# Optimization experiments

Measured on AMD Instinct MI355X. Metric: run time of the kernel, lower is better.

Reference implementation:

```python
import jax, jax.numpy as jnp
import numpy as np

DIM = 512; NH = 8; HD = DIM // NH; WS = 28; N = WS * WS; H3 = (DIM * 4) // 3; EPS = 1e-6; B = 16


def _rel_pos_index(H, W):
    # static numpy computation of Swin-style relative position index [N, N]
    coords = np.stack(np.meshgrid(np.arange(H), np.arange(W), indexing='ij')).reshape(2, -1)
    rel = (coords[:, :, None] - coords[:, None, :]).transpose(1, 2, 0)
    rel[..., 0] += H - 1
    rel[..., 1] += W - 1
    rel[..., 0] *= 2 * W - 1
    return rel.sum(-1)

RPI = jnp.asarray(_rel_pos_index(WS, WS))  # [N, N] int


def adaptive_ln(x, w, b, a1w, a1b, a2w, a2b):
    # x: [B,C,H,W]; adapt params from global-avg-pooled 1x1 convs (== matmuls)
    C = x.shape[1]
    pooled = x.mean(axis=(2, 3))                      # [B,C]
    h = jax.nn.relu(pooled @ a1w.T + a1b)             # [B,C/4]
    ad = h @ a2w.T + a2b                              # [B,2C]
    aw = ad[:, :C][:, :, None, None]
    ab = ad[:, C:][:, :, None, None]
    u = x.mean(axis=1, keepdims=True)
    s = ((x - u) ** 2).mean(axis=1, keepdims=True)
    xn = (x - u) * jax.lax.rsqrt(s + EPS)
    return (w[None, :, None, None] * (1.0 + aw)) * xn + (b[None, :, None, None] + ab)


def dwconv(x, w, b):
    y = jax.lax.conv_general_dilated(x, w, (1, 1), 'SAME', feature_group_count=x.shape[1],
                                     dimension_numbers=('NCHW', 'OIHW', 'NCHW'))
    return y + b[None, :, None, None]


def conv1x1(x, w, b):
    return jnp.einsum('bchw,oc->bohw', x, w) + b[None, :, None, None]


def _forward(x, face_priors, n1_w, n1_b, n1_a1w, n1_a1b, n1_a2w, n1_a2b,
             n2_w, n2_b, n2_a1w, n2_a1b, n2_a2w, n2_a2b,
             qkv_w, qkv_b, rpb_table, struct_prior, proj_w, proj_b,
             eye_w, eye_b, nose_w, nose_b, mouth_w, mouth_b,
             fusion_w, fusion_b, gate1_w, gate1_b, gate2_w, gate2_b,
             es1_w, es1_b, es2_w, es2_b, em1_w, em1_b, em2_w, em2_b,
             el1_w, el1_b, el2_w, el2_b, router_w, router_b):
    Bx, C, H, W = x.shape
    n = H * W
    shortcut = x
    xa = adaptive_ln(x, n1_w, n1_b, n1_a1w, n1_a1b, n1_a2w, n1_a2b)
    # --- TripletFaceAttention ---
    xf = xa.reshape(Bx, C, n).transpose(0, 2, 1)                     # [B,N,C]
    qkv = (xf @ qkv_w.T + qkv_b).reshape(Bx, n, 3, NH, HD).transpose(2, 0, 3, 1, 4)
    q, k, v = qkv[0], qkv[1], qkv[2]                                 # [B,h,N,d]
    attn = jnp.einsum('bhnd,bhmd->bhnm', q, k) * (HD ** -0.5)
    attn = attn + struct_prior                                       # learned structure prior [1,h,N,N]
    rpb = rpb_table[RPI]                                             # [N,N,h]
    attn = attn + jnp.transpose(rpb, (2, 0, 1))[None]                # + relative position bias
    attn = attn * face_priors[:, None]                               # multiplicative face mask
    attn = jax.nn.softmax(attn, axis=-1)
    o = jnp.einsum('bhnm,bhmd->bhnd', attn, v).transpose(0, 2, 1, 3).reshape(Bx, n, C)
    o = o @ proj_w.T + proj_b
    x = shortcut + o.transpose(0, 2, 1).reshape(Bx, C, H, W)
    # --- FaceTokenMixer ---
    xn2 = adaptive_ln(x, n2_w, n2_b, n2_a1w, n2_a1b, n2_a2w, n2_a2b)
    cat = jnp.concatenate([dwconv(xn2, eye_w, eye_b),
                           dwconv(xn2, nose_w, nose_b),
                           dwconv(xn2, mouth_w, mouth_b)], axis=1)   # [B,3C,H,W]
    g = jax.nn.sigmoid(conv1x1(jax.nn.relu(conv1x1(xn2, gate1_w, gate1_b)), gate2_w, gate2_b))
    x = x + conv1x1(cat * g, fusion_w, fusion_b)
    # --- EfficientMLP (3-expert MoE, soft routing) ---
    r = jax.nn.softmax(x.mean(axis=(2, 3)) @ router_w.T + router_b, axis=-1)  # [B,3]
    def expert(w1, b1, w2, b2):
        return conv1x1(jax.nn.gelu(conv1x1(x, w1, b1), approximate=False), w2, b2)
    out = (r[:, 0, None, None, None] * expert(es1_w, es1_b, es2_w, es2_b)
           + r[:, 1, None, None, None] * expert(em1_w, em1_b, em2_w, em2_b)
           + r[:, 2, None, None, None] * expert(el1_w, el1_b, el2_w, el2_b))
    return x + out


def setup_inputs() -> dict:
    ks = iter(jax.random.split(jax.random.key(0), 64))
    def rn(shape, s=0.02):
        return jax.random.normal(next(ks), shape, jnp.float32) * s
    d = {}
    d['x'] = jax.random.normal(next(ks), (B, DIM, WS, WS), jnp.float32)
    d['face_priors'] = jax.random.uniform(next(ks), (B, N, N), jnp.float32)
    for p in ('n1', 'n2'):
        d[p + '_w'] = jnp.ones((DIM,), jnp.float32)
        d[p + '_b'] = jnp.zeros((DIM,), jnp.float32)
        d[p + '_a1w'] = rn((DIM // 4, DIM)); d[p + '_a1b'] = jnp.zeros((DIM // 4,), jnp.float32)
        d[p + '_a2w'] = rn((2 * DIM, DIM // 4)); d[p + '_a2b'] = jnp.zeros((2 * DIM,), jnp.float32)
    d['qkv_w'] = rn((3 * DIM, DIM)); d['qkv_b'] = jnp.zeros((3 * DIM,), jnp.float32)
    d['rpb_table'] = rn(((2 * WS - 1) ** 2, NH))
    d['struct_prior'] = rn((1, NH, N, N))
    d['proj_w'] = rn((DIM, DIM)); d['proj_b'] = jnp.zeros((DIM,), jnp.float32)
    d['eye_w'] = rn((DIM, 1, 3, 3)); d['eye_b'] = jnp.zeros((DIM,), jnp.float32)
    d['nose_w'] = rn((DIM, 1, 5, 5)); d['nose_b'] = jnp.zeros((DIM,), jnp.float32)
    d['mouth_w'] = rn((DIM, 1, 7, 7)); d['mouth_b'] = jnp.zeros((DIM,), jnp.float32)
    d['fusion_w'] = rn((DIM, 3 * DIM)); d['fusion_b'] = jnp.zeros((DIM,), jnp.float32)
    d['gate1_w'] = rn((DIM // 4, DIM)); d['gate1_b'] = jnp.zeros((DIM // 4,), jnp.float32)
    d['gate2_w'] = rn((3 * DIM, DIM // 4)); d['gate2_b'] = jnp.zeros((3 * DIM,), jnp.float32)
    for e in ('es', 'em', 'el'):
        d[e + '1_w'] = rn((H3, DIM)); d[e + '1_b'] = jnp.zeros((H3,), jnp.float32)
        d[e + '2_w'] = rn((DIM, H3)); d[e + '2_b'] = jnp.zeros((DIM,), jnp.float32)
    d['router_w'] = rn((3, DIM)); d['router_b'] = jnp.zeros((3,), jnp.float32)
    return d


def reference(x, face_priors, n1_w, n1_b, n1_a1w, n1_a1b, n1_a2w, n1_a2b,
              n2_w, n2_b, n2_a1w, n2_a1b, n2_a2w, n2_a2b,
              qkv_w, qkv_b, rpb_table, struct_prior, proj_w, proj_b,
              eye_w, eye_b, nose_w, nose_b, mouth_w, mouth_b,
              fusion_w, fusion_b, gate1_w, gate1_b, gate2_w, gate2_b,
              es1_w, es1_b, es2_w, es2_b, em1_w, em1_b, em2_w, em2_b,
              el1_w, el1_b, el2_w, el2_b, router_w, router_b):
    return _forward(x, face_priors, n1_w, n1_b, n1_a1w, n1_a1b, n1_a2w, n1_a2b,
                    n2_w, n2_b, n2_a1w, n2_a1b, n2_a2w, n2_a2b,
                    qkv_w, qkv_b, rpb_table, struct_prior, proj_w, proj_b,
                    eye_w, eye_b, nose_w, nose_b, mouth_w, mouth_b,
                    fusion_w, fusion_b, gate1_w, gate1_b, gate2_w, gate2_b,
                    es1_w, es1_b, es2_w, es2_b, em1_w, em1_b, em2_w, em2_b,
                    el1_w, el1_b, el2_w, el2_b, router_w, router_b)
```

## Files before the change

### kernel.cpp

```cpp
#include <hip/hip_runtime.h>
#include <math.h>


#define NPIX 784
#define CDIM 512
#define NHEAD 8
#define C3 1536

typedef unsigned int uint;
typedef unsigned short ushort;
typedef float f32x4 __attribute__((ext_vector_type(4)));
typedef __bf16 bf16x8 __attribute__((ext_vector_type(8)));

#define OFF_XPM ((size_t)0)
#define OFF_W   ((size_t)3211264)
#define OFF_R2  ((size_t)5324288)
#define OFF_VBF ((size_t)14958080)
#define OFF_OBF ((size_t)18169344)
#define OFF_X2  ((size_t)21380608)
#define OFF_X3  ((size_t)27803136)
#define OFF_PL  ((size_t)34225664)
#define OFF_AD  ((size_t)34233856)
#define OFF_RB  ((size_t)34250240)
#define OFF_US  ((size_t)34250288)
#define OFF_RS  ((size_t)34262832)

#define WOFF_QKV 0
#define WOFF_PROJ 786432
#define WOFF_G1  1048576
#define WOFF_G2  1114112
#define WOFF_FUS 1310720
#define WOFF_E1  2097152
#define WOFF_E2  3144704

__device__ __forceinline__ ushort f2bf(float f) {
  unsigned u = __builtin_bit_cast(unsigned, f);
  unsigned r = (u + 0x7fffu + ((u >> 16) & 1u)) >> 16;
  return (ushort)r;
}
__device__ __forceinline__ unsigned pack2bf(float lo, float hi) {
  return (unsigned)f2bf(lo) | ((unsigned)f2bf(hi) << 16);
}
__device__ __forceinline__ float bf2f(ushort u) {
  unsigned x = ((unsigned)u) << 16;
  return __builtin_bit_cast(float, x);
}
__device__ __forceinline__ void unpack4bf(uint2 v, float* o) {
  o[0] = bf2f((ushort)(v.x & 0xffffu)); o[1] = bf2f((ushort)(v.x >> 16));
  o[2] = bf2f((ushort)(v.y & 0xffffu)); o[3] = bf2f((ushort)(v.y >> 16));
}

__global__ __launch_bounds__(64) void pool_mean_k(const float* __restrict__ x,
                                                  float* __restrict__ pooled) {
  int c = blockIdx.x, b = blockIdx.y;
  const float* row = x + ((size_t)b * CDIM + c) * NPIX;
  float s = 0.f;
  for (int i = threadIdx.x; i < NPIX; i += 64) s += row[i];
  #pragma unroll
  for (int off = 32; off; off >>= 1) s += __shfl_down(s, off);
  if (threadIdx.x == 0) pooled[b * CDIM + c] = s * (1.f / NPIX);
}

__global__ __launch_bounds__(256) void adapt_mlp_k(const float* __restrict__ pooled,
                                                   const float* __restrict__ a1w,
                                                   const float* __restrict__ a1b,
                                                   const float* __restrict__ a2w,
                                                   const float* __restrict__ a2b,
                                                   float* __restrict__ ad) {
  int b = blockIdx.x, tid = threadIdx.x;
  __shared__ float pl[CDIM];
  __shared__ float hh[128];
  for (int i = tid; i < CDIM; i += 256) pl[i] = pooled[b * CDIM + i];
  __syncthreads();
  if (tid < 128) {
    const float* w = a1w + (size_t)tid * CDIM;
    float a = a1b[tid];
    for (int k = 0; k < CDIM; ++k) a += w[k] * pl[k];
    hh[tid] = fmaxf(a, 0.f);
  }
  __syncthreads();
  for (int o = tid; o < 1024; o += 256) {
    const float* w = a2w + (size_t)o * 128;
    float a = a2b[o];
    for (int k = 0; k < 128; ++k) a += w[k] * hh[k];
    ad[b * 1024 + o] = a;
  }
}

template <int STATS>
__global__ __launch_bounds__(256) void ln_pm_k(const float* __restrict__ x,
                                               const float* __restrict__ w,
                                               const float* __restrict__ bias,
                                               const float* __restrict__ ad,
                                               ushort* __restrict__ out,
                                               float* __restrict__ ust,
                                               float* __restrict__ rstp) {
  int b = blockIdx.y;
  int p0 = blockIdx.x * 32;
  int tid = threadIdx.x;
  int px = tid & 31, cg = tid >> 5;
  int p = p0 + px;
  bool valid = p < NPIX;
  const float* xb = x + (size_t)b * CDIM * NPIX;
  float s = 0.f, s2 = 0.f;
  if (valid) {
    for (int c = cg * 64; c < cg * 64 + 64; ++c) {
      float v = xb[(size_t)c * NPIX + p];
      s += v; s2 += v * v;
    }
  }
  __shared__ float rs[8][32], rq[8][32], us[32], vs[32];
  rs[cg][px] = s; rq[cg][px] = s2;
  __syncthreads();
  if (tid < 32) {
    float ts = 0.f, ts2 = 0.f;
    #pragma unroll
    for (int g = 0; g < 8; ++g) { ts += rs[g][tid]; ts2 += rq[g][tid]; }
    float u = ts * (1.f / CDIM);
    float var = ts2 * (1.f / CDIM) - u * u;
    float rv = rsqrtf(var + 1e-6f);
    us[tid] = u; vs[tid] = rv;
    if (STATS && p0 + tid < NPIX) {
      ust[(size_t)b * NPIX + p0 + tid] = u;
      rstp[(size_t)b * NPIX + p0 + tid] = rv;
    }
  }
  __syncthreads();
  if (valid) {
    float u = us[px], rv = vs[px];
    const float* aw = ad + (size_t)b * 1024;
    const float* ab = aw + CDIM;
    ushort* ob = out + ((size_t)(b * NPIX + p)) * CDIM + cg * 64;
    for (int cb = 0; cb < 64; cb += 8) {
      int c = cg * 64 + cb;
      float vv[8];
      #pragma unroll
      for (int q = 0; q < 8; ++q) {
        float v = xb[(size_t)(c + q) * NPIX + p];
        vv[q] = w[c + q] * (1.f + aw[c + q]) * ((v - u) * rv) + (bias[c + q] + ab[c + q]);
      }
      uint4 o = {pack2bf(vv[0], vv[1]), pack2bf(vv[2], vv[3]),
                 pack2bf(vv[4], vv[5]), pack2bf(vv[6], vv[7])};
      *(uint4*)(ob + cb) = o;
    }
  }
}

struct CvtDesc {
  const float* s[11];
  ushort* d[11];
  int rows[11], sk[11], dk[11];
};
__global__ __launch_bounds__(256) void cvt_w_k(CvtDesc D) {
  int seg = blockIdx.y;
  int sk = D.sk[seg], dk = D.dk[seg];
  int total = D.rows[seg] * dk;
  const float* s = D.s[seg];
  ushort* d = D.d[seg];
  for (int i = blockIdx.x * 256 + threadIdx.x; i < total; i += gridDim.x * 256) {
    int r = i / dk, cc = i - r * dk;
    d[i] = (cc < sk) ? f2bf(s[(size_t)r * sk + cc]) : (ushort)0;
  }
}

__global__ __launch_bounds__(256) void sprpb_k(const float* __restrict__ sp,
                                               const float* __restrict__ rpb,
                                               ushort* __restrict__ out) {
  const int q = blockIdx.x, h = blockIdx.y;
  const int i1 = q / 28, j1 = q - i1 * 28;
  const float* src = sp + ((size_t)h * NPIX + q) * NPIX;
  ushort* dst = out + ((size_t)h * NPIX + q) * NPIX;
  for (int m = threadIdx.x; m < NPIX; m += 256) {
    int i2 = m / 28, j2 = m - i2 * 28;
    float rv = rpb[(size_t)((i1 - i2 + 27) * 55 + (j1 - j2 + 27)) * NHEAD + h];
    dst[m] = f2bf(src[m] + rv);
  }
}

__global__ __launch_bounds__(256) void fpcvt_k(const float* __restrict__ fp,
                                               ushort* __restrict__ out) {
  size_t i = (size_t)blockIdx.x * 256 + threadIdx.x;
  float4 v = *((const float4*)fp + i);
  ushort4 o;
  o.x = f2bf(v.x); o.y = f2bf(v.y); o.z = f2bf(v.z); o.w = f2bf(v.w);
  *((ushort4*)out + i) = o;
}

template <int ORIENT, int EPI>
__global__ __launch_bounds__(256) void mgemm_k(const ushort* __restrict__ X,
                                               const ushort* __restrict__ Wt,
                                               const float* __restrict__ bias,
                                               const float* __restrict__ resid,
                                               const float* __restrict__ scales,
                                               void* __restrict__ OutV,
                                               int Ks, int Nreal, int Nstore) {
  const int b = blockIdx.z;
  const int m0 = blockIdx.x * 112;
  const int n0 = blockIdx.y * 128;
  const int t = threadIdx.x;
  const int w = t >> 6, lane = t & 63, c = lane & 15, g = lane >> 4;
  __shared__ ushort Xs[7168];
  __shared__ ushort Ws[8192];
  f32x4 acc[7][2];
  #pragma unroll
  for (int mi = 0; mi < 7; ++mi)
    #pragma unroll
    for (int ni = 0; ni < 2; ++ni) acc[mi][ni] = (f32x4){0.f, 0.f, 0.f, 0.f};

  const ushort* Xb = X + (size_t)b * NPIX * Ks;
  for (int k0 = 0; k0 < Ks; k0 += 64) {
    for (int i = t; i < 896; i += 256) {
      int m = i >> 3, kg = i & 7;
      uint4 v = *(const uint4*)(Xb + (size_t)(m0 + m) * Ks + k0 + kg * 8);
      *(uint4*)&Xs[m * 64 + ((kg ^ (m & 7)) << 3)] = v;
    }
    for (int i = t; i < 1024; i += 256) {
      int n = i >> 3, kg = i & 7;
      uint4 v = {0u, 0u, 0u, 0u};
      if (n0 + n < Nreal) v = *(const uint4*)(Wt + (size_t)(n0 + n) * Ks + k0 + kg * 8);
      *(uint4*)&Ws[n * 64 + ((kg ^ (n & 7)) << 3)] = v;
    }
    __syncthreads();
    #pragma unroll
    for (int kc = 0; kc < 2; ++kc) {
      bf16x8 xf[7], wf[2];
      #pragma unroll
      for (int mi = 0; mi < 7; ++mi) {
        int m = mi * 16 + c;
        xf[mi] = *(const bf16x8*)&Xs[m * 64 + (((kc * 4 + g) ^ (m & 7)) << 3)];
      }
      #pragma unroll
      for (int ni = 0; ni < 2; ++ni) {
        int n = w * 32 + ni * 16 + c;
        wf[ni] = *(const bf16x8*)&Ws[n * 64 + (((kc * 4 + g) ^ (n & 7)) << 3)];
      }
      #pragma unroll
      for (int mi = 0; mi < 7; ++mi)
        #pragma unroll
        for (int ni = 0; ni < 2; ++ni)
          acc[mi][ni] = (ORIENT == 0)
            ? __builtin_amdgcn_mfma_f32_16x16x32_bf16(wf[ni], xf[mi], acc[mi][ni], 0, 0, 0)
            : __builtin_amdgcn_mfma_f32_16x16x32_bf16(xf[mi], wf[ni], acc[mi][ni], 0, 0, 0);
    }
    __syncthreads();
  }

  if (ORIENT == 0) {
    ushort* Ob = (ushort*)OutV + (size_t)b * NPIX * Nstore;
    const int nbq = n0 + w * 32;
    float bi[2][4];
    #pragma unroll
    for (int ni = 0; ni < 2; ++ni)
      #pragma unroll
      for (int j = 0; j < 4; ++j) {
        int n = nbq + ni * 16 + g * 4 + j;
        bi[ni][j] = (n < Nreal) ? bias[n] : 0.f;
      }
    #pragma unroll
    for (int mi = 0; mi < 7; ++mi) {
      int m = m0 + mi * 16 + c;
      #pragma unroll
      for (int ni = 0; ni < 2; ++ni) {
        int nb = nbq + ni * 16 + g * 4;
        if (nb >= Nstore) continue;
        float v[4];
        #pragma unroll
        for (int j = 0; j < 4; ++j) v[j] = acc[mi][ni][j] + bi[ni][j];
        if (EPI == 1) {
          #pragma unroll
          for (int j = 0; j < 4; ++j) v[j] = fmaxf(v[j], 0.f);
        } else if (EPI == 2) {
          #pragma unroll
          for (int j = 0; j < 4; ++j)
            v[j] = 0.5f * v[j] * (1.f + erff(v[j] * 0.70710678118654752f));
        } else if (EPI == 3) {
          uint2 cm = *(const uint2*)&Ob[(size_t)m * Nstore + nb];
          float cf[4];
          unpack4bf(cm, cf);
          #pragma unroll
          for (int j = 0; j < 4; ++j)
            v[j] = (1.f / (1.f + __expf(-v[j]))) * cf[j];
        }
        uint2 o = {pack2bf(v[0], v[1]), pack2bf(v[2], v[3])};
        *(uint2*)&Ob[(size_t)m * Nstore + nb] = o;
      }
    }
  } else {
    float* Ob = (float*)OutV + (size_t)b * CDIM * NPIX;
    const float* Rb = resid + (size_t)b * CDIM * NPIX;
    float sc = scales ? scales[b * 3] : 1.f;
    #pragma unroll
    for (int ni = 0; ni < 2; ++ni) {
      int n = n0 + w * 32 + ni * 16 + c;
      float bv = bias[n];
      #pragma unroll
      for (int mi = 0; mi < 7; ++mi) {
        int m = m0 + mi * 16 + g * 4;
        size_t off = (size_t)n * NPIX + m;
        float4 r = *(const float4*)&Rb[off];
        f32x4 a = acc[mi][ni];
        float4 o = {r.x + sc * (a[0] + bv), r.y + sc * (a[1] + bv),
                    r.z + sc * (a[2] + bv), r.w + sc * (a[3] + bv)};
        *(float4*)&Ob[off] = o;
      }
    }
  }
}

__global__ __launch_bounds__(256) void vtr_k(const ushort* __restrict__ qkvbf,
                                             ushort* __restrict__ vbf) {
  const int p0 = blockIdx.x * 64, c0 = blockIdx.y * 64, b = blockIdx.z;
  __shared__ ushort T[64][72];
  for (int idx = threadIdx.x; idx < 512; idx += 256) {
    int pl = idx >> 3, cq = idx & 7;
    int p = p0 + pl;
    uint4 v = {0u, 0u, 0u, 0u};
    if (p < NPIX)
      v = *(const uint4*)(qkvbf + (size_t)(b * NPIX + p) * C3 + 1024 + c0 + cq * 8);
    *(uint4*)&T[pl][cq * 8] = v;
  }
  __syncthreads();
  for (int idx = threadIdx.x; idx < 512; idx += 256) {
    int cl = idx >> 3, pq = idx & 7;
    if (p0 + pq * 8 < NPIX) {
      ushort tmp[8];
      #pragma unroll
      for (int i = 0; i < 8; ++i) tmp[i] = T[pq * 8 + i][cl];
      *(uint4*)(vbf + ((size_t)(b * CDIM + c0 + cl)) * NPIX + p0 + pq * 8) =
          *(const uint4*)&tmp[0];
    }
  }
}

__global__ __launch_bounds__(256) void tr_cvt_k(const float* __restrict__ src,
                                                ushort* __restrict__ dst) {
  const int p0 = blockIdx.x * 64, c0 = blockIdx.y * 64, b = blockIdx.z;
  __shared__ ushort T[64][72];
  const float* sb = src + (size_t)b * CDIM * NPIX;
  for (int idx = threadIdx.x; idx < 4096; idx += 256) {
    int ci = idx >> 6, pj = idx & 63;
    int p = p0 + pj;
    T[pj][ci] = (p < NPIX) ? f2bf(sb[(size_t)(c0 + ci) * NPIX + p]) : (ushort)0;
  }
  __syncthreads();
  for (int idx = threadIdx.x; idx < 512; idx += 256) {
    int pj = idx >> 3, cq = idx & 7;
    int p = p0 + pj;
    if (p < NPIX) {
      uint4 v = *(const uint4*)&T[pj][cq * 8];
      *(uint4*)(dst + ((size_t)(b * NPIX + p)) * CDIM + c0 + cq * 8) = v;
    }
  }
}

__global__ __launch_bounds__(256) void attn_mfma_k(const ushort* __restrict__ qkvbf,
                                                   const ushort* __restrict__ vbf,
                                                   const ushort* __restrict__ sprpb,
                                                   const ushort* __restrict__ fpb,
                                                   ushort* __restrict__ obf) {
  const int h = blockIdx.y, b = blockIdx.z;
  const int w = threadIdx.x >> 6, lane = threadIdx.x & 63;
  const int g = lane >> 4, c = lane & 15;
  const int q0 = blockIdx.x * 128 + w * 32;
  if (q0 >= NPIX) return;
  const bool hasB = (q0 + 16) < NPIX;
  const int qA = q0 + c;
  const int qB = q0 + 16 + c;

  __shared__ uint BL[4][2][384];
  uint* bwA = BL[w][0];
  uint* bwB = BL[w][1];

  const ushort* qpA = qkvbf + (size_t)(b * NPIX + qA) * C3 + h * 64 + g * 8;
  const bf16x8 qfA0 = *(const bf16x8*)qpA;
  const bf16x8 qfA1 = *(const bf16x8*)(qpA + 32);
  bf16x8 qfB0 = qfA0, qfB1 = qfA1;
  if (hasB) {
    const ushort* qpB = qkvbf + (size_t)(b * NPIX + qB) * C3 + h * 64 + g * 8;
    qfB0 = *(const bf16x8*)qpB;
    qfB1 = *(const bf16x8*)(qpB + 32);
  }

  const ushort* kbase = qkvbf + (size_t)b * NPIX * C3 + 512 + h * 64 + g * 8;
  const ushort* vbase = vbf + ((size_t)b * CDIM + h * 64) * NPIX;
  const ushort* sprA = sprpb + ((size_t)h * NPIX + qA) * NPIX;
  const ushort* sprB = sprpb + ((size_t)h * NPIX + (hasB ? qB : qA)) * NPIX;
  const ushort* fpA = fpb + ((size_t)b * NPIX + qA) * NPIX;
  const ushort* fpB = fpb + ((size_t)b * NPIX + (hasB ? qB : qA)) * NPIX;

  f32x4 oA0 = {0.f, 0.f, 0.f, 0.f}, oA1 = oA0, oA2 = oA0, oA3 = oA0;
  f32x4 oB0 = oA0, oB1 = oA0, oB2 = oA0, oB3 = oA0;
  float MA = -1e30f, LA = 0.f, MB = -1e30f, LB = 0.f;

  for (int ms = 0; ms < 25; ++ms) {
    const int m0 = ms * 32;
    const bool full = (ms < 24);

    const ushort* kp = kbase + (size_t)(m0 + c) * C3;
    bf16x8 ka0 = *(const bf16x8*)kp;
    bf16x8 ka1 = *(const bf16x8*)(kp + 32);
    bf16x8 kb0 = ka0, kb1 = ka1;
    if (full) {
      const ushort* kp1 = kp + (size_t)16 * C3;
      kb0 = *(const bf16x8*)kp1;
      kb1 = *(const bf16x8*)(kp1 + 32);
    }

    f32x4 sA0 = {0.f, 0.f, 0.f, 0.f}, sA1 = sA0;
    sA0 = __builtin_amdgcn_mfma_f32_16x16x32_bf16(ka0, qfA0, sA0, 0, 0, 0);
    sA0 = __builtin_amdgcn_mfma_f32_16x16x32_bf16(ka1, qfA1, sA0, 0, 0, 0);
    if (full) {
      sA1 = __builtin_amdgcn_mfma_f32_16x16x32_bf16(kb0, qfA0, sA1, 0, 0, 0);
      sA1 = __builtin_amdgcn_mfma_f32_16x16x32_bf16(kb1, qfA1, sA1, 0, 0, 0);
    }

    float vA0[4], vA1[4];
    {
      float spv[4], fpv[4];
      unpack4bf(*(const uint2*)(sprA + m0 + g * 4), spv);
      unpack4bf(*(const uint2*)(fpA + m0 + g * 4), fpv);
      #pragma unroll
      for (int j = 0; j < 4; ++j) vA0[j] = fmaf(sA0[j], 0.125f, spv[j]) * fpv[j];
      if (full) {
        unpack4bf(*(const uint2*)(sprA + m0 + 16 + g * 4), spv);
        unpack4bf(*(const uint2*)(fpA + m0 + 16 + g * 4), fpv);
        #pragma unroll
        for (int j = 0; j < 4; ++j) vA1[j] = fmaf(sA1[j], 0.125f, spv[j]) * fpv[j];
      }
    }
    {
      float tm = fmaxf(fmaxf(vA0[0], vA0[1]), fmaxf(vA0[2], vA0[3]));
      if (full) tm = fmaxf(tm, fmaxf(fmaxf(vA1[0], vA1[1]), fmaxf(vA1[2], vA1[3])));
      tm = fmaxf(tm, __shfl_xor(tm, 16));
      tm = fmaxf(tm, __shfl_xor(tm, 32));
      const float nM = fmaxf(MA, tm);
      const float fac = __expf(MA - nM);
      float p0v[4], p1v[4];
      float ps = 0.f;
      #pragma unroll
      for (int j = 0; j < 4; ++j) { p0v[j] = __expf(vA0[j] - nM); ps += p0v[j]; }
      if (full) {
        #pragma unroll
        for (int j = 0; j < 4; ++j) { p1v[j] = __expf(vA1[j] - nM); ps += p1v[j]; }
      }
      ps += __shfl_xor(ps, 16);
      ps += __shfl_xor(ps, 32);
      LA = LA * fac + ps;
      MA = nM;
      #pragma unroll
      for (int j = 0; j < 4; ++j) { oA0[j] *= fac; oA1[j] *= fac; oA2[j] *= fac; oA3[j] *= fac; }
      uint2 wlo, whi;
      wlo.x = pack2bf(p0v[0], p0v[1]);
      wlo.y = pack2bf(p0v[2], p0v[3]);
      whi.x = full ? pack2bf(p1v[0], p1v[1]) : 0u;
      whi.y = full ? pack2bf(p1v[2], p1v[3]) : 0u;
      *(uint2*)&bwA[lane * 6] = wlo;
      *(uint2*)&bwA[lane * 6 + 2] = whi;
    }

    if (hasB) {
      f32x4 sB0 = {0.f, 0.f, 0.f, 0.f}, sB1 = sB0;
      sB0 = __builtin_amdgcn_mfma_f32_16x16x32_bf16(ka0, qfB0, sB0, 0, 0, 0);
      sB0 = __builtin_amdgcn_mfma_f32_16x16x32_bf16(ka1, qfB1, sB0, 0, 0, 0);
      if (full) {
        sB1 = __builtin_amdgcn_mfma_f32_16x16x32_bf16(kb0, qfB0, sB1, 0, 0, 0);
        sB1 = __builtin_amdgcn_mfma_f32_16x16x32_bf16(kb1, qfB1, sB1, 0, 0, 0);
      }
      float vB0[4], vB1[4];
      {
        float spv[4], fpv[4];
        unpack4bf(*(const uint2*)(sprB + m0 + g * 4), spv);
        unpack4bf(*(const uint2*)(fpB + m0 + g * 4), fpv);
        #pragma unroll
        for (int j = 0; j < 4; ++j) vB0[j] = fmaf(sB0[j], 0.125f, spv[j]) * fpv[j];
        if (full) {
          unpack4bf(*(const uint2*)(sprB + m0 + 16 + g * 4), spv);
          unpack4bf(*(const uint2*)(fpB + m0 + 16 + g * 4), fpv);
          #pragma unroll
          for (int j = 0; j < 4; ++j) vB1[j] = fmaf(sB1[j], 0.125f, spv[j]) * fpv[j];
        }
      }
      float tm = fmaxf(fmaxf(vB0[0], vB0[1]), fmaxf(vB0[2], vB0[3]));
      if (full) tm = fmaxf(tm, fmaxf(fmaxf(vB1[0], vB1[1]), fmaxf(vB1[2], vB1[3])));
      tm = fmaxf(tm, __shfl_xor(tm, 16));
      tm = fmaxf(tm, __shfl_xor(tm, 32));
      const float nM = fmaxf(MB, tm);
      const float fac = __expf(MB - nM);
      float p0v[4], p1v[4];
      float ps = 0.f;
      #pragma unroll
      for (int j = 0; j < 4; ++j) { p0v[j] = __expf(vB0[j] - nM); ps += p0v[j]; }
      if (full) {
        #pragma unroll
        for (int j = 0; j < 4; ++j) { p1v[j] = __expf(vB1[j] - nM); ps += p1v[j]; }
      }
      ps += __shfl_xor(ps, 16);
      ps += __shfl_xor(ps, 32);
      LB = LB * fac + ps;
      MB = nM;
      #pragma unroll
      for (int j = 0; j < 4; ++j) { oB0[j] *= fac; oB1[j] *= fac; oB2[j] *= fac; oB3[j] *= fac; }
      uint2 wlo, whi;
      wlo.x = pack2bf(p0v[0], p0v[1]);
      wlo.y = pack2bf(p0v[2], p0v[3]);
      whi.x = full ? pack2bf(p1v[0], p1v[1]) : 0u;
      whi.y = full ? pack2bf(p1v[2], p1v[3]) : 0u;
      *(uint2*)&bwB[lane * 6] = wlo;
      *(uint2*)&bwB[lane * 6 + 2] = whi;
    }

    const int f = g >> 1;
    const int slo = 32 * (g & 1) + c;
    uint2 blo = *(const uint2*)&bwA[slo * 6 + f * 2];
    uint2 bhi = *(const uint2*)&bwA[(slo + 16) * 6 + f * 2];
    uint4 bba = {blo.x, blo.y, bhi.x, bhi.y};
    const bf16x8 pfA = __builtin_bit_cast(bf16x8, bba);

    const ushort* vp = vbase + (size_t)c * NPIX + m0 + g * 8;
    bf16x8 vf0 = *(const bf16x8*)(vp);
    bf16x8 vf1 = *(const bf16x8*)(vp + (size_t)16 * NPIX);
    bf16x8 vf2 = *(const bf16x8*)(vp + (size_t)32 * NPIX);
    bf16x8 vf3 = *(const bf16x8*)(vp + (size_t)48 * NPIX);
    oA0 = __builtin_amdgcn_mfma_f32_16x16x32_bf16(vf0, pfA, oA0, 0, 0, 0);
    oA1 = __builtin_amdgcn_mfma_f32_16x16x32_bf16(vf1, pfA, oA1, 0, 0, 0);
    oA2 = __builtin_amdgcn_mfma_f32_16x16x32_bf16(vf2, pfA, oA2, 0, 0, 0);
    oA3 = __builtin_amdgcn_mfma_f32_16x16x32_bf16(vf3, pfA, oA3, 0, 0, 0);
    if (hasB) {
      uint2 clo = *(const uint2*)&bwB[slo * 6 + f * 2];
      uint2 chi = *(const uint2*)&bwB[(slo + 16) * 6 + f * 2];
      uint4 bbb = {clo.x, clo.y, chi.x, chi.y};
      const bf16x8 pfB = __builtin_bit_cast(bf16x8, bbb);
      oB0 = __builtin_amdgcn_mfma_f32_16x16x32_bf16(vf0, pfB, oB0, 0, 0, 0);
      oB1 = __builtin_amdgcn_mfma_f32_16x16x32_bf16(vf1, pfB, oB1, 0, 0, 0);
      oB2 = __builtin_amdgcn_mfma_f32_16x16x32_bf16(vf2, pfB, oB2, 0, 0, 0);
      oB3 = __builtin_amdgcn_mfma_f32_16x16x32_bf16(vf3, pfB, oB3, 0, 0, 0);
    }
  }

  {
    const float invL = 1.f / LA;
    ushort* dst = obf + (size_t)(b * NPIX + qA) * CDIM + h * 64 + g * 4;
    f32x4 ot[4] = {oA0, oA1, oA2, oA3};
    #pragma unroll
    for (int t2 = 0; t2 < 4; ++t2) {
      uint2 o = {pack2bf(ot[t2][0] * invL, ot[t2][1] * invL),
                 pack2bf(ot[t2][2] * invL, ot[t2][3] * invL)};
      *(uint2*)(dst + t2 * 16) = o;
    }
  }
  if (hasB) {
    const float invL = 1.f / LB;
    ushort* dst = obf + (size_t)(b * NPIX + qB) * CDIM + h * 64 + g * 4;
    f32x4 ot[4] = {oB0, oB1, oB2, oB3};
    #pragma unroll
    for (int t2 = 0; t2 < 4; ++t2) {
      uint2 o = {pack2bf(ot[t2][0] * invL, ot[t2][1] * invL),
                 pack2bf(ot[t2][2] * invL, ot[t2][3] * invL)};
      *(uint2*)(dst + t2 * 16) = o;
    }
  }
}

__device__ __forceinline__ float bf2f_s(ushort u) { return bf2f(u); }

template <int R>
__device__ __forceinline__ void conv_pass(const ushort* __restrict__ plane_ci,
                                          const float* __restrict__ wl_ci,
                                          float bv, int slot,
                                          ushort (*__restrict__ outb)[16], int ci) {
  constexpr int K = 2 * R + 1;
  float wreg[K * K];
  #pragma unroll
  for (int i = 0; i < K * K; ++i) wreg[i] = wl_ci[i];
  #pragma unroll
  for (int r7 = 0; r7 < 7; ++r7) {
    const int run = slot + r7 * 16;
    const int y = run >> 2, x0 = (run & 3) * 7;
    float acc[7];
    #pragma unroll
    for (int i = 0; i < 7; ++i) acc[i] = bv;
    #pragma unroll
    for (int dy = 0; dy < K; ++dy) {
      const ushort* rp = plane_ci + (y + 3 - R + dy) * 34 + (x0 + 3 - R);
      float win[7 + 2 * R];
      #pragma unroll
      for (int k = 0; k < 7 + 2 * R; ++k) win[k] = bf2f_s(rp[k]);
      #pragma unroll
      for (int i = 0; i < 7; ++i)
        #pragma unroll
        for (int k = 0; k < K; ++k)
          acc[i] = fmaf(win[i + k], wreg[dy * K + k], acc[i]);
    }
    #pragma unroll
    for (int i = 0; i < 7; ++i) outb[y * 28 + x0 + i][ci] = f2bf(acc[i]);
  }
}

__global__ __launch_bounds__(256) void dwln_k(const float* __restrict__ x2,
    const float* __restrict__ ust, const float* __restrict__ rst,
    const float* __restrict__ ad, const float* __restrict__ n2w,
    const float* __restrict__ n2b,
    const float* __restrict__ ew, const float* __restrict__ eb,
    const float* __restrict__ nw, const float* __restrict__ nb,
    const float* __restrict__ mw, const float* __restrict__ mb,
    ushort* __restrict__ cat) {
  const int cg = blockIdx.x, b = blockIdx.y;
  const int c0 = cg * 16;
  const int t = threadIdx.x;
  const int ci = t & 15, slot = t >> 4;

  __shared__ ushort plane[16][1156];
  __shared__ ushort outb[784][16];
  __shared__ float Wl[16 * 49];
  __shared__ float LWs[16], LBs[16];

  {
    uint* pz = (uint*)&plane[0][0];
    for (int i = t; i < 16 * 1156 / 2; i += 256) pz[i] = 0u;
  }
  if (t < 16) {
    int cc = c0 + t;
    float aw = ad[b * 1024 + cc], ab = ad[b * 1024 + 512 + cc];
    LWs[t] = n2w[cc] * (1.f + aw);
    LBs[t] = n2b[cc] + ab;
  }
  __syncthreads();

  {
    float uu[4], rr[4];
    #pragma unroll
    for (int j = 0; j < 4; ++j) {
      int p = t + j * 256;
      if (p < NPIX) {
        uu[j] = ust[(size_t)b * NPIX + p];
        rr[j] = rst[(size_t)b * NPIX + p];
      }
    }
    for (int cc = 0; cc < 16; ++cc) {
      const float* xp = x2 + ((size_t)(b * CDIM + c0 + cc)) * NPIX;
      float lw = LWs[cc], lb = LBs[cc];
      #pragma unroll
      for (int j = 0; j < 4; ++j) {
        int p = t + j * 256;
        if (p < NPIX) {
          int y = p / 28, xx2 = p - y * 28;
          plane[cc][(y + 3) * 34 + xx2 + 3] = f2bf(lw * (xp[p] - uu[j]) * rr[j] + lb);
        }
      }
    }
  }
  __syncthreads();

  #pragma unroll 1
  for (int cv = 0; cv < 3; ++cv) {
    const float* gw = (cv == 0) ? ew : (cv == 1) ? nw : mw;
    const float* gb = (cv == 0) ? eb : (cv == 1) ? nb : mb;
    const int K2 = (cv == 0) ? 9 : (cv == 1) ? 25 : 49;
    for (int i = t; i < 16 * K2; i += 256) {
      int cc = i / K2, k = i - cc * K2;
      Wl[cc * K2 + k] = gw[(size_t)(c0 + cc) * K2 + k];
    }
    __syncthreads();
    float bv = gb[c0 + ci];
    if (cv == 0)      conv_pass<1>(&plane[ci][0], &Wl[ci * 9],  bv, slot, outb, ci);
    else if (cv == 1) conv_pass<2>(&plane[ci][0], &Wl[ci * 25], bv, slot, outb, ci);
    else              conv_pass<3>(&plane[ci][0], &Wl[ci * 49], bv, slot, outb, ci);
    __syncthreads();
    for (int idx = t; idx < NPIX * 2; idx += 256) {
      int p = idx >> 1, half = idx & 1;
      uint4 v = *(const uint4*)&outb[p][half * 8];
      *(uint4*)(cat + ((size_t)(b * NPIX + p)) * C3 + cv * 512 + c0 + half * 8) = v;
    }
    __syncthreads();
  }
}

__global__ __launch_bounds__(64) void router_k(const float* __restrict__ pooled,
                                               const float* __restrict__ rw,
                                               const float* __restrict__ rb,
                                               float* __restrict__ r) {
  int b = blockIdx.x, lane = threadIdx.x;
  float a0 = 0.f, a1 = 0.f, a2 = 0.f;
  for (int k = lane; k < CDIM; k += 64) {
    float p = pooled[b * CDIM + k];
    a0 += rw[k] * p;
    a1 += rw[CDIM + k] * p;
    a2 += rw[2 * CDIM + k] * p;
  }
  #pragma unroll
  for (int off = 32; off; off >>= 1) {
    a0 += __shfl_down(a0, off);
    a1 += __shfl_down(a1, off);
    a2 += __shfl_down(a2, off);
  }
  if (lane == 0) {
    float l0 = a0 + rb[0], l1 = a1 + rb[1], l2 = a2 + rb[2];
    float mx = fmaxf(l0, fmaxf(l1, l2));
    float e0 = __expf(l0 - mx), e1 = __expf(l1 - mx), e2 = __expf(l2 - mx);
    float inv = 1.f / (e0 + e1 + e2);
    r[b * 3 + 0] = e0 * inv;
    r[b * 3 + 1] = e1 * inv;
    r[b * 3 + 2] = e2 * inv;
  }
}

extern "C" void kernel_launch(void* const* d_in, const int* in_sizes, int n_in,
                              void* d_out, int out_size, void* d_ws, size_t ws_size,
                              hipStream_t stream) {
  (void)in_sizes; (void)n_in; (void)out_size; (void)ws_size;
  const float* x         = (const float*)d_in[0];
  const float* fpri      = (const float*)d_in[1];
  const float* n1_w      = (const float*)d_in[2];
  const float* n1_b      = (const float*)d_in[3];
  const float* n1_a1w    = (const float*)d_in[4];
  const float* n1_a1b    = (const float*)d_in[5];
  const float* n1_a2w    = (const float*)d_in[6];
  const float* n1_a2b    = (const float*)d_in[7];
  const float* n2_w      = (const float*)d_in[8];
  const float* n2_b      = (const float*)d_in[9];
  const float* n2_a1w    = (const float*)d_in[10];
  const float* n2_a1b    = (const float*)d_in[11];
  const float* n2_a2w    = (const float*)d_in[12];
  const float* n2_a2b    = (const float*)d_in[13];
  const float* qkv_w     = (const float*)d_in[14];
  const float* qkv_b     = (const float*)d_in[15];
  const float* rpb_table = (const float*)d_in[16];
  const float* sprior    = (const float*)d_in[17];
  const float* proj_w    = (const float*)d_in[18];
  const float* proj_b    = (const float*)d_in[19];
  const float* eye_w     = (const float*)d_in[20];
  const float* eye_b     = (const float*)d_in[21];
  const float* nose_w    = (const float*)d_in[22];
  const float* nose_b    = (const float*)d_in[23];
  const float* mouth_w   = (const float*)d_in[24];
  const float* mouth_b   = (const float*)d_in[25];
  const float* fusion_w  = (const float*)d_in[26];
  const float* fusion_b  = (const float*)d_in[27];
  const float* gate1_w   = (const float*)d_in[28];
  const float* gate1_b   = (const float*)d_in[29];
  const float* gate2_w   = (const float*)d_in[30];
  const float* gate2_b   = (const float*)d_in[31];
  const float* e1w[3] = {(const float*)d_in[32], (const float*)d_in[36], (const float*)d_in[40]};
  const float* e1b[3] = {(const float*)d_in[33], (const float*)d_in[37], (const float*)d_in[41]};
  const float* e2w[3] = {(const float*)d_in[34], (const float*)d_in[38], (const float*)d_in[42]};
  const float* e2b[3] = {(const float*)d_in[35], (const float*)d_in[39], (const float*)d_in[43]};
  const float* router_w  = (const float*)d_in[44];
  const float* router_b  = (const float*)d_in[45];

  float* ws    = (float*)d_ws;
  ushort* xpm  = (ushort*)(ws + OFF_XPM);
  ushort* wb   = (ushort*)(ws + OFF_W);
  ushort* r2u  = (ushort*)(ws + OFF_R2);
  ushort* vbf  = (ushort*)(ws + OFF_VBF);
  ushort* obf  = (ushort*)(ws + OFF_OBF);
  float* x2    = ws + OFF_X2;
  float* x3    = ws + OFF_X3;
  float* pld   = ws + OFF_PL;
  float* adb   = ws + OFF_AD;
  float* rbuf  = ws + OFF_RB;
  float* ust   = ws + OFF_US;
  float* rst   = ws + OFF_RS;
  float* outp  = (float*)d_out;

  ushort* qkvw = wb + WOFF_QKV;
  ushort* projw = wb + WOFF_PROJ;
  ushort* g1w  = wb + WOFF_G1;
  ushort* g2w  = wb + WOFF_G2;
  ushort* fusw = wb + WOFF_FUS;

  ushort* fpbf   = (ushort*)x2;
  ushort* sprpbf = (ushort*)x3;

  CvtDesc D;
  D.s[0] = qkv_w;    D.d[0] = qkvw;  D.rows[0] = 1536; D.sk[0] = 512;  D.dk[0] = 512;
  D.s[1] = proj_w;   D.d[1] = projw; D.rows[1] = 512;  D.sk[1] = 512;  D.dk[1] = 512;
  D.s[2] = gate1_w;  D.d[2] = g1w;   D.rows[2] = 128;  D.sk[2] = 512;  D.dk[2] = 512;
  D.s[3] = gate2_w;  D.d[3] = g2w;   D.rows[3] = 1536; D.sk[3] = 128;  D.dk[3] = 128;
  D.s[4] = fusion_w; D.d[4] = fusw;  D.rows[4] = 512;  D.sk[4] = 1536; D.dk[4] = 1536;
  for (int e = 0; e < 3; ++e) {
    D.s[5 + e] = e1w[e]; D.d[5 + e] = wb + WOFF_E1 + e * 349184;
    D.rows[5 + e] = 682; D.sk[5 + e] = 512; D.dk[5 + e] = 512;
    D.s[8 + e] = e2w[e]; D.d[8 + e] = wb + WOFF_E2 + e * 360448;
    D.rows[8 + e] = 512; D.sk[8 + e] = 682; D.dk[8 + e] = 704;
  }
  cvt_w_k<<<dim3(512, 11), 256, 0, stream>>>(D);

  sprpb_k<<<dim3(NPIX, NHEAD), 256, 0, stream>>>(sprior, rpb_table, sprpbf);
  fpcvt_k<<<9604, 256, 0, stream>>>(fpri, fpbf);

  pool_mean_k<<<dim3(CDIM, 16), 64, 0, stream>>>(x, pld);
  adapt_mlp_k<<<16, 256, 0, stream>>>(pld, n1_a1w, n1_a1b, n1_a2w, n1_a2b, adb);
  ln_pm_k<0><<<dim3(25, 16), 256, 0, stream>>>(x, n1_w, n1_b, adb, xpm, nullptr, nullptr);

  mgemm_k<0, 0><<<dim3(7, 12, 16), 256, 0, stream>>>(xpm, qkvw, qkv_b, nullptr, nullptr,
                                                     r2u, 512, 1536, 1536);
  vtr_k<<<dim3(13, 8, 16), 256, 0, stream>>>(r2u, vbf);
  attn_mfma_k<<<dim3(7, 8, 16), 256, 0, stream>>>(r2u, vbf, sprpbf, fpbf, obf);
  mgemm_k<1, 4><<<dim3(7, 4, 16), 256, 0, stream>>>(obf, projw, proj_b, x, nullptr,
                                                    x2, 512, 512, 512);

  pool_mean_k<<<dim3(CDIM, 16), 64, 0, stream>>>(x2, pld);
  adapt_mlp_k<<<16, 256, 0, stream>>>(pld, n2_a1w, n2_a1b, n2_a2w, n2_a2b, adb);
  ln_pm_k<1><<<dim3(25, 16), 256, 0, stream>>>(x2, n2_w, n2_b, adb, xpm, ust, rst);
  dwln_k<<<dim3(32, 16), 256, 0, stream>>>(x2, ust, rst, adb, n2_w, n2_b,
                                           eye_w, eye_b, nose_w, nose_b, mouth_w, mouth_b,
                                           r2u);
  mgemm_k<0, 1><<<dim3(7, 1, 16), 256, 0, stream>>>(xpm, g1w, gate1_b, nullptr, nullptr,
                                                    obf, 512, 128, 128);
  mgemm_k<0, 3><<<dim3(7, 12, 16), 256, 0, stream>>>(obf, g2w, gate2_b, nullptr, nullptr,
                                                     r2u, 128, 1536, 1536);
  mgemm_k<1, 4><<<dim3(7, 4, 16), 256, 0, stream>>>(r2u, fusw, fusion_b, x2, nullptr,
                                                    x3, 1536, 512, 512);

  tr_cvt_k<<<dim3(13, 8, 16), 256, 0, stream>>>(x3, vbf);
  pool_mean_k<<<dim3(CDIM, 16), 64, 0, stream>>>(x3, pld);
  router_k<<<16, 64, 0, stream>>>(pld, router_w, router_b, rbuf);
  for (int e = 0; e < 3; ++e) {
    mgemm_k<0, 2><<<dim3(7, 6, 16), 256, 0, stream>>>(vbf, wb + WOFF_E1 + e * 349184,
                                                      e1b[e], nullptr, nullptr,
                                                      r2u, 512, 682, 704);
    mgemm_k<1, 4><<<dim3(7, 4, 16), 256, 0, stream>>>(r2u, wb + WOFF_E2 + e * 360448,
                                                      e2b[e], (e == 0) ? x3 : outp,
                                                      rbuf + e, outp, 704, 512, 512);
  }
}
```

Measured before the change: 902.6 us.

## Remap GEMM and attention blocks to 1D grid with XCD-aware tile assignment

Flattens the GEMM grid so the batch dimension is folded into M (MTOT rows), and assigns contiguous M tiles to the same XCD via bid&7 swizzling. The attention kernel likewise maps each batch to a fixed XCD so its K/V data is shared in that XCD's L2. The goal is better L2 locality across MI355X's chiplets, at the cost of extra index arithmetic and a hardcoded tile count (14 M-tiles per XCD).

```diff
diff --git a/kernel.cpp b/kernel.cpp
--- a/kernel.cpp
+++ b/kernel.cpp
@@ -6,6 +6,7 @@
 #define CDIM 512
 #define NHEAD 8
 #define C3 1536
+#define MTOT 12544
 
 typedef unsigned int uint;
 typedef unsigned short ushort;
@@ -194,9 +195,13 @@
                                                const float* __restrict__ scales,
                                                void* __restrict__ OutV,
                                                int Ks, int Nreal, int Nstore) {
-  const int b = blockIdx.z;
-  const int m0 = blockIdx.x * 112;
-  const int n0 = blockIdx.y * 128;
+  const int bid = blockIdx.x;
+  const int xcd = bid & 7;
+  const int i = bid >> 3;
+  const int mt_local = i % 14;
+  const int nt = i / 14;
+  const int m0 = (xcd * 14 + mt_local) * 112;
+  const int n0 = nt * 128;
   const int t = threadIdx.x;
   const int w = t >> 6, lane = t & 63, c = lane & 15, g = lane >> 4;
   __shared__ ushort Xs[7168];
@@ -207,15 +212,14 @@
     #pragma unroll
     for (int ni = 0; ni < 2; ++ni) acc[mi][ni] = (f32x4){0.f, 0.f, 0.f, 0.f};
 
-  const ushort* Xb = X + (size_t)b * NPIX * Ks;
   for (int k0 = 0; k0 < Ks; k0 += 64) {
-    for (int i = t; i < 896; i += 256) {
-      int m = i >> 3, kg = i & 7;
-      uint4 v = *(const uint4*)(Xb + (size_t)(m0 + m) * Ks + k0 + kg * 8);
+    for (int ii = t; ii < 896; ii += 256) {
+      int m = ii >> 3, kg = ii & 7;
+      uint4 v = *(const uint4*)(X + (size_t)(m0 + m) * Ks + k0 + kg * 8);
       *(uint4*)&Xs[m * 64 + ((kg ^ (m & 7)) << 3)] = v;
     }
-    for (int i = t; i < 1024; i += 256) {
-      int n = i >> 3, kg = i & 7;
+    for (int ii = t; ii < 1024; ii += 256) {
+      int n = ii >> 3, kg = ii & 7;
       uint4 v = {0u, 0u, 0u, 0u};
       if (n0 + n < Nreal) v = *(const uint4*)(Wt + (size_t)(n0 + n) * Ks + k0 + kg * 8);
       *(uint4*)&Ws[n * 64 + ((kg ^ (n & 7)) << 3)] = v;
@@ -246,7 +250,7 @@
   }
 
   if (ORIENT == 0) {
-    ushort* Ob = (ushort*)OutV + (size_t)b * NPIX * Nstore;
+    ushort* Ob = (ushort*)OutV;
     const int nbq = n0 + w * 32;
     float bi[2][4];
     #pragma unroll
@@ -286,17 +290,19 @@
       }
     }
   } else {
-    float* Ob = (float*)OutV + (size_t)b * CDIM * NPIX;
-    const float* Rb = resid + (size_t)b * CDIM * NPIX;
-    float sc = scales ? scales[b * 3] : 1.f;
+    const int bb = m0 / NPIX;
+    const int prow = m0 - bb * NPIX;
+    float* Ob = (float*)OutV + (size_t)bb * CDIM * NPIX;
+    const float* Rb = resid + (size_t)bb * CDIM * NPIX;
+    float sc = scales ? scales[bb * 3] : 1.f;
     #pragma unroll
     for (int ni = 0; ni < 2; ++ni) {
       int n = n0 + w * 32 + ni * 16 + c;
       float bv = bias[n];
       #pragma unroll
       for (int mi = 0; mi < 7; ++mi) {
-        int m = m0 + mi * 16 + g * 4;
-        size_t off = (size_t)n * NPIX + m;
+        int p = prow + mi * 16 + g * 4;
+        size_t off = (size_t)n * NPIX + p;
         float4 r = *(const float4*)&Rb[off];
         f32x4 a = acc[mi][ni];
         float4 o = {r.x + sc * (a[0] + bv), r.y + sc * (a[1] + bv),
@@ -358,10 +364,16 @@
                                                    const ushort* __restrict__ sprpb,
                                                    const ushort* __restrict__ fpb,
                                                    ushort* __restrict__ obf) {
-  const int h = blockIdx.y, b = blockIdx.z;
+  const int bid = blockIdx.x;
+  const int xcd = bid & 7;
+  const int i = bid >> 3;
+  const int b = xcd + 8 * (i / 56);
+  const int r = i % 56;
+  const int h = r & 7;
+  const int qt = r >> 3;
   const int w = threadIdx.x >> 6, lane = threadIdx.x & 63;
   const int g = lane >> 4, c = lane & 15;
-  const int q0 = blockIdx.x * 128 + w * 32;
+  const int q0 = qt * 128 + w * 32;
   if (q0 >= NPIX) return;
   const bool hasB = (q0 + 16) < NPIX;
   const int qA = q0 + c;
@@ -792,12 +804,12 @@
   adapt_mlp_k<<<16, 256, 0, stream>>>(pld, n1_a1w, n1_a1b, n1_a2w, n1_a2b, adb);
   ln_pm_k<0><<<dim3(25, 16), 256, 0, stream>>>(x, n1_w, n1_b, adb, xpm, nullptr, nullptr);
 
-  mgemm_k<0, 0><<<dim3(7, 12, 16), 256, 0, stream>>>(xpm, qkvw, qkv_b, nullptr, nullptr,
-                                                     r2u, 512, 1536, 1536);
+  mgemm_k<0, 0><<<1344, 256, 0, stream>>>(xpm, qkvw, qkv_b, nullptr, nullptr,
+                                          r2u, 512, 1536, 1536);
   vtr_k<<<dim3(13, 8, 16), 256, 0, stream>>>(r2u, vbf);
-  attn_mfma_k<<<dim3(7, 8, 16), 256, 0, stream>>>(r2u, vbf, sprpbf, fpbf, obf);
-  mgemm_k<1, 4><<<dim3(7, 4, 16), 256, 0, stream>>>(obf, projw, proj_b, x, nullptr,
-                                                    x2, 512, 512, 512);
+  attn_mfma_k<<<896, 256, 0, stream>>>(r2u, vbf, sprpbf, fpbf, obf);
+  mgemm_k<1, 4><<<448, 256, 0, stream>>>(obf, projw, proj_b, x, nullptr,
+                                         x2, 512, 512, 512);
 
   pool_mean_k<<<dim3(CDIM, 16), 64, 0, stream>>>(x2, pld);
   adapt_mlp_k<<<16, 256, 0, stream>>>(pld, n2_a1w, n2_a1b, n2_a2w, n2_a2b, adb);
@@ -805,22 +817,22 @@
   dwln_k<<<dim3(32, 16), 256, 0, stream>>>(x2, ust, rst, adb, n2_w, n2_b,
                                            eye_w, eye_b, nose_w, nose_b, mouth_w, mouth_b,
                                            r2u);
-  mgemm_k<0, 1><<<dim3(7, 1, 16), 256, 0, stream>>>(xpm, g1w, gate1_b, nullptr, nullptr,
-                                                    obf, 512, 128, 128);
-  mgemm_k<0, 3><<<dim3(7, 12, 16), 256, 0, stream>>>(obf, g2w, gate2_b, nullptr, nullptr,
-                                                     r2u, 128, 1536, 1536);
-  mgemm_k<1, 4><<<dim3(7, 4, 16), 256, 0, stream>>>(r2u, fusw, fusion_b, x2, nullptr,
-                                                    x3, 1536, 512, 512);
+  mgemm_k<0, 1><<<112, 256, 0, stream>>>(xpm, g1w, gate1_b, nullptr, nullptr,
+                                         obf, 512, 128, 128);
+  mgemm_k<0, 3><<<1344, 256, 0, stream>>>(obf, g2w, gate2_b, nullptr, nullptr,
+                                          r2u, 128, 1536, 1536);
+  mgemm_k<1, 4><<<448, 256, 0, stream>>>(r2u, fusw, fusion_b, x2, nullptr,
+                                         x3, 1536, 512, 512);
 
   tr_cvt_k<<<dim3(13, 8, 16), 256, 0, stream>>>(x3, vbf);
   pool_mean_k<<<dim3(CDIM, 16), 64, 0, stream>>>(x3, pld);
   router_k<<<16, 64, 0, stream>>>(pld, router_w, router_b, rbuf);
   for (int e = 0; e < 3; ++e) {
-    mgemm_k<0, 2><<<dim3(7, 6, 16), 256, 0, stream>>>(vbf, wb + WOFF_E1 + e * 349184,
-                                                      e1b[e], nullptr, nullptr,
-                                                      r2u, 512, 682, 704);
-    mgemm_k<1, 4><<<dim3(7, 4, 16), 256, 0, stream>>>(r2u, wb + WOFF_E2 + e * 360448,
-                                                      e2b[e], (e == 0) ? x3 : outp,
-                                                      rbuf + e, outp, 704, 512, 512);
-  }
-}
+    mgemm_k<0, 2><<<672, 256, 0, stream>>>(vbf, wb + WOFF_E1 + e * 349184,
+                                           e1b[e], nullptr, nullptr,
+                                           r2u, 512, 682, 704);
+    mgemm_k<1, 4><<<448, 256, 0, stream>>>(r2u, wb + WOFF_E2 + e * 360448,
+                                           e2b[e], (e == 0) ? x3 : outp,
+                                           rbuf + e, outp, 704, 512, 512);
+  }
+}
```

After: 862.4 us. -4.4%, faster.
